# Performance work log

Measured on AMD Instinct MI355X. Metric: run time of the kernel, lower is better.

Reference implementation:

```python
import jax, jax.numpy as jnp
import numpy as np

D_MODEL = 2048
NUM_HEADS = 16
HEAD_DIM = D_MODEL // NUM_HEADS  # 128; scale uses head_dim even though attention is over full d_model
B, S = 2, 2048


def setup_inputs() -> dict:
    key = jax.random.key(0)
    ks = jax.random.split(key, 5)
    x = jax.random.normal(ks[0], (B, S, D_MODEL), dtype=jnp.float32)
    # causal additive mask, as typically passed to this module (2D, sliced mask[-s:, :kv])
    neg = jnp.float32(-1e9)
    mask = jnp.where(jnp.triu(jnp.ones((S, S), dtype=bool), k=1), neg, jnp.float32(0.0))
    std = 1.0 / np.sqrt(D_MODEL)
    Wq = jax.random.normal(ks[1], (D_MODEL, D_MODEL), dtype=jnp.float32) * std
    Wk = jax.random.normal(ks[2], (D_MODEL, D_MODEL), dtype=jnp.float32) * std
    Wv = jax.random.normal(ks[3], (D_MODEL, D_MODEL), dtype=jnp.float32) * std
    Wo = jax.random.normal(ks[4], (D_MODEL, D_MODEL), dtype=jnp.float32) * std
    return {"x": x, "mask": mask, "Wq": Wq, "Wk": Wk, "Wv": Wv, "Wo": Wo}


def reference(x, mask, Wq, Wk, Wv, Wo):
    # nn.Linear(bias=False): y = x @ W^T
    q = jnp.einsum('bsd,ed->bse', x, Wq)  # [B,S,D]
    k = jnp.einsum('bsd,ed->bse', x, Wk)
    v = jnp.einsum('bsd,ed->bse', x, Wv)
    scale = jnp.float32(HEAD_DIM ** -0.5)
    # NOTE: faithful to source — contraction over full d_model, no head split
    scores = jnp.einsum('bsd,btd->bst', q, k) * scale  # [B,S,S]
    scores = scores + mask  # mask[-s:, :kv] == mask here (s == kv)
    weights = jax.nn.softmax(scores, axis=-1)
    out = jnp.einsum('bst,btd->bsd', weights, v)
    return jnp.einsum('bsd,ed->bse', out, Wo)
```

## Files before the change

### kernel.cpp

```cpp
#include <hip/hip_runtime.h>

#define DM  2048
#define SQ  2048
#define NB  2
#define BSZ (NB * SQ)

typedef _Float16 f16x8 __attribute__((ext_vector_type(8)));
typedef __attribute__((ext_vector_type(4))) float f32x4;

#define ASG(p) (const __attribute__((address_space(1))) void*)(p)
#define ASL(p) (__attribute__((address_space(3))) void*)(p)

__device__ __forceinline__ unsigned short f2h(float f) {
  union { _Float16 h; unsigned short u; } x;
  x.h = (_Float16)f;
  return x.u;
}
__device__ __forceinline__ float h2f(unsigned short u) {
  union { unsigned short u; _Float16 h; } x;
  x.u = u;
  return (float)x.h;
}

__global__ __launch_bounds__(256) void cast_x_wo(const float4* __restrict__ x,
                                                 const float4* __restrict__ wo,
                                                 ushort4* __restrict__ outx,
                                                 ushort4* __restrict__ outwo,
                                                 int n4x, int n4w) {
  int i = blockIdx.x * 256 + threadIdx.x;
  float4 v;
  ushort4* dst;
  int j;
  if (i < n4x) { v = x[i]; dst = outx; j = i; }
  else { j = i - n4x; if (j >= n4w) return; v = wo[j]; dst = outwo; }
  ushort4 h;
  h.x = f2h(v.x); h.y = f2h(v.y); h.z = f2h(v.z); h.w = f2h(v.w);
  dst[j] = h;
}

__global__ __launch_bounds__(256) void cast_t(const float* __restrict__ wq,
                                              const float* __restrict__ wk,
                                              const float* __restrict__ wv,
                                              unsigned short* __restrict__ wqT,
                                              unsigned short* __restrict__ wkT,
                                              unsigned short* __restrict__ wvT) {
  __shared__ unsigned short tile[64][66];
  const float* in = (blockIdx.z == 0) ? wq : (blockIdx.z == 1) ? wk : wv;
  unsigned short* outT = (blockIdx.z == 0) ? wqT : (blockIdx.z == 1) ? wkT : wvT;
  const int tid = threadIdx.x;
  const int d0 = blockIdx.x * 64, e0 = blockIdx.y * 64;
  const int r = tid >> 4;
  const int c = (tid & 15) * 4;
#pragma unroll
  for (int p = 0; p < 4; p++) {
    const int dl = r + p * 16;
    float4 v = *(const float4*)&in[(long)(d0 + dl) * DM + e0 + c];
    tile[c + 0][dl] = f2h(v.x);
    tile[c + 1][dl] = f2h(v.y);
    tile[c + 2][dl] = f2h(v.z);
    tile[c + 3][dl] = f2h(v.w);
  }
  __syncthreads();
  const int r2 = tid >> 3;
  const int c2 = (tid & 7) * 8;
#pragma unroll
  for (int p = 0; p < 2; p++) {
    const int el = r2 + p * 32;
    union { uint4 u4; unsigned short us[8]; } o;
#pragma unroll
    for (int k = 0; k < 8; k++) o.us[k] = tile[el][c2 + k];
    *(uint4*)&outT[(long)(e0 + el) * DM + d0 + c2] = o.u4;
  }
}

#define SB() __builtin_amdgcn_sched_barrier(0)
#define BARX() do { SB(); __builtin_amdgcn_s_barrier(); SB(); } while (0)

#define STAGEK(BUFL, REG, U, T) do { \
    const unsigned short* G_ = (REG) ? Bb : Ab; \
    const int ldG_ = (REG) ? ldB : ldA; \
    const int r0_ = ((REG) ? bn0 : bm0) + (U) * 32; \
    const long k0_ = (long)((T) << 6); \
    char* db_ = ldsb + (BUFL) * 32768 + (REG) * 16384 + (U) * 4096 + tid * 16; \
    const unsigned short* s_ = G_ + (long)(r0_ + srow) * ldG_ + k0_ + scsw; \
    __builtin_amdgcn_global_load_lds(ASG(s_), ASL(db_), 16, 0, 0); \
  } while (0)

#define LDAK(BUFL, MH, Af) do { \
    const char* ba_ = ldsb + (BUFL) * 32768 + (wm * 64 + (MH) * 32) * 128 + arow; \
    _Pragma("unroll") for (int mm_ = 0; mm_ < 2; mm_++) { \
      Af[mm_][0] = *(const f16x8*)(ba_ + mm_ * 2048 + sl0); \
      Af[mm_][1] = *(const f16x8*)(ba_ + mm_ * 2048 + sl1); } \
  } while (0)

#define LDBK(BUFL, NH, Bf) do { \
    const char* bb_ = ldsb + (BUFL) * 32768 + 16384 + (wn * 64 + (NH) * 32) * 128 + arow; \
    _Pragma("unroll") for (int nn_ = 0; nn_ < 2; nn_++) { \
      Bf[nn_][0] = *(const f16x8*)(bb_ + nn_ * 2048 + sl0); \
      Bf[nn_][1] = *(const f16x8*)(bb_ + nn_ * 2048 + sl1); } \
  } while (0)

#define PHK(Af, Bf, MH, NH) do { \
    __builtin_amdgcn_s_setprio(1); \
    _Pragma("unroll") for (int mm_ = 0; mm_ < 2; mm_++) \
    _Pragma("unroll") for (int nn_ = 0; nn_ < 2; nn_++) \
    _Pragma("unroll") for (int ks_ = 0; ks_ < 2; ks_++) \
      acc[(MH) * 2 + mm_][(NH) * 2 + nn_] = __builtin_amdgcn_mfma_f32_16x16x32_f16( \
          Af[mm_][ks_], Bf[nn_][ks_], acc[(MH) * 2 + mm_][(NH) * 2 + nn_], 0, 0, 0); \
    __builtin_amdgcn_s_setprio(0); \
  } while (0)

#define GROUPK(BUFL, T) do { \
    LDAK(BUFL, 0, a0); LDBK(BUFL, 0, b0); \
    LDAK(BUFL, 1, a1); \
    if ((T) + 1 < NT) { STAGEK((BUFL) ^ 1, 1, 2, (T) + 1); STAGEK((BUFL) ^ 1, 1, 3, (T) + 1); } \
    PHK(a0, b0, 0, 0); \
    BARX(); \
    LDBK(BUFL, 1, b1); \
    PHK(a1, b0, 1, 0); \
    BARX(); \
    if ((T) + 2 < NT) { STAGEK(BUFL, 0, 0, (T) + 2); STAGEK(BUFL, 0, 1, (T) + 2); \
                        STAGEK(BUFL, 0, 2, (T) + 2); STAGEK(BUFL, 0, 3, (T) + 2); } \
    PHK(a1, b1, 1, 1); \
    BARX(); \
    if ((T) + 2 < NT) { STAGEK(BUFL, 1, 0, (T) + 2); STAGEK(BUFL, 1, 1, (T) + 2); } \
    PHK(a0, b1, 0, 1); \
    SB(); \
    if ((T) + 1 < NT) { \
      if ((T) + 1 == NT - 1) { asm volatile("s_waitcnt vmcnt(0)" ::: "memory"); } \
      else                   { asm volatile("s_waitcnt vmcnt(6)" ::: "memory"); } \
    } \
    __builtin_amdgcn_s_barrier(); \
    SB(); \
  } while (0)

template <int OM>
__device__ __forceinline__ void gemm128_body(
    char* ldsb, const unsigned short* __restrict__ Ab,
    const unsigned short* __restrict__ Bb,
    float* __restrict__ Cf, unsigned short* __restrict__ Ch, long cb,
    int NT, int ldA, int ldB, int ldC, int bm0, int bn0, float alpha) {
  const int tid = threadIdx.x, lane = tid & 63, wid = tid >> 6;
  const int wm = wid >> 1, wn = wid & 1;
  const int fr = lane & 15, fq = lane >> 4;

  const int sl0 = ((fq ^ (fr & 7)) << 4);
  const int sl1 = (((4 + fq) ^ (fr & 7)) << 4);
  const int arow = fr << 7;

  const int srow = tid >> 3;
  const int scsw = ((tid & 7) ^ (srow & 7)) << 3;

  f32x4 acc[4][4];
#pragma unroll
  for (int m = 0; m < 4; m++)
#pragma unroll
    for (int n = 0; n < 4; n++)
#pragma unroll
      for (int r = 0; r < 4; r++) acc[m][n][r] = 0.f;

  f16x8 a0[2][2], a1[2][2], b0[2][2], b1[2][2];

  STAGEK(0, 0, 0, 0); STAGEK(0, 0, 1, 0); STAGEK(0, 0, 2, 0); STAGEK(0, 0, 3, 0);
  STAGEK(0, 1, 0, 0); STAGEK(0, 1, 1, 0); STAGEK(0, 1, 2, 0); STAGEK(0, 1, 3, 0);
  STAGEK(1, 0, 0, 1); STAGEK(1, 0, 1, 1); STAGEK(1, 0, 2, 1); STAGEK(1, 0, 3, 1);
  STAGEK(1, 1, 0, 1); STAGEK(1, 1, 1, 1);
  asm volatile("s_waitcnt vmcnt(6)" ::: "memory");
  __builtin_amdgcn_s_barrier();
  SB();

  for (int t = 0; t < NT; t += 2) {
    GROUPK(0, t);
    GROUPK(1, t + 1);
  }

#pragma unroll
  for (int mh = 0; mh < 2; mh++)
#pragma unroll
    for (int mm = 0; mm < 2; mm++)
#pragma unroll
      for (int nh = 0; nh < 2; nh++)
#pragma unroll
        for (int nn = 0; nn < 2; nn++) {
          const int col = bn0 + wn * 64 + nh * 32 + nn * 16 + fr;
#pragma unroll
          for (int r = 0; r < 4; r++) {
            const long row = (long)bm0 + wm * 64 + mh * 32 + mm * 16 + fq * 4 + r;
            const long ci = cb + row * ldC + col;
            const float vv = acc[mh * 2 + mm][nh * 2 + nn][r] * alpha;
            if constexpr (OM == 0) Cf[ci] = vv;
            else                   Ch[ci] = f2h(vv);
          }
        }
}

template <int OM, int CAUSAL>
__global__ __launch_bounds__(256, 2) void gemm128(
    const unsigned short* __restrict__ A, const unsigned short* __restrict__ B,
    float* __restrict__ Cf, unsigned short* __restrict__ Ch,
    int K, long sAb, long sBb, long sCb,
    int ldA, int ldB, int ldC, float alpha) {
  __shared__ __align__(16) char ldsarr[65536];
  const int bm0 = blockIdx.x * 128;
  const int bn0 = blockIdx.y * 128;
  if (CAUSAL == 1 && bn0 > bm0) return;
  const int z = blockIdx.z;
  gemm128_body<OM>(ldsarr, A + (long)z * sAb, B + (long)z * sBb,
                   Cf, Ch, (long)z * sCb, K >> 6, ldA, ldB, ldC, bm0, bn0, alpha);
}

__global__ __launch_bounds__(256, 2) void k_mt_g(
    const unsigned short* __restrict__ wkT, const unsigned short* __restrict__ wqT,
    const unsigned short* __restrict__ wo16, const unsigned short* __restrict__ wvT,
    unsigned short* __restrict__ MT, unsigned short* __restrict__ G) {
  __shared__ __align__(16) char ldsarr[65536];
  const int bm0 = blockIdx.x * 128;
  const int bn0 = blockIdx.y * 128;
  if (blockIdx.z == 0)
    gemm128_body<1>(ldsarr, wkT, wqT, nullptr, MT, 0L, DM >> 6, DM, DM, DM, bm0, bn0, 1.0f);
  else
    gemm128_body<1>(ldsarr, wo16, wvT, nullptr, G, 0L, DM >> 6, DM, DM, DM, bm0, bn0, 1.0f);
}

__global__ __launch_bounds__(256, 2) void k_y_ut(
    const unsigned short* __restrict__ x16, const unsigned short* __restrict__ MT,
    const unsigned short* __restrict__ G,
    unsigned short* __restrict__ y, unsigned short* __restrict__ uT) {
  __shared__ __align__(16) char ldsarr[65536];
  if (blockIdx.z == 0) {
    const int bm0 = blockIdx.x * 128;
    const int bn0 = blockIdx.y * 128;
    gemm128_body<1>(ldsarr, x16, MT, nullptr, y, 0L, DM >> 6, DM, DM, DM, bm0, bn0, 1.0f);
  } else {
    const int bm0 = blockIdx.y * 128;
    const int bn0 = blockIdx.x * 128;
    gemm128_body<1>(ldsarr, G, x16, nullptr, uT, 0L, DM >> 6, DM, DM, BSZ, bm0, bn0, 1.0f);
  }
}

__global__ __launch_bounds__(256, 2) void k_out(
    const unsigned short* __restrict__ probs, const unsigned short* __restrict__ uT,
    float* __restrict__ out) {
  __shared__ __align__(16) char ldsarr[65536];
  const int x = blockIdx.x;
  const int bn0 = blockIdx.y * 128;
  const long z = blockIdx.z & 1;
  const int row = (blockIdx.z >> 1) ? (15 - x) : x;
  const unsigned short* Ab = probs + z * (long)SQ * SQ;
  const unsigned short* Bb = uT + z * 2048;
  gemm128_body<0>(ldsarr, Ab, Bb, out, nullptr, z * (long)SQ * DM,
                  2 * (row + 1), SQ, BSZ, DM, 128 * row, bn0, 1.0f);
}

__global__ __launch_bounds__(256) void softmax_causal(const unsigned short* __restrict__ sc,
                                                      unsigned short* __restrict__ pr) {
  const int row = blockIdx.x;
  const int s = row & (SQ - 1);
  const long base = (long)row * SQ;
  const int n = s + 1;
  const int tid = threadIdx.x;
  const int lane = tid & 63;
  const int wv = tid >> 6;
  const int e0 = tid * 8;
  __shared__ float red[4];

  union { uint4 u4; unsigned short us[8]; } in, ou;
  in.u4 = *(const uint4*)&sc[base + e0];

  float v[8];
  float mx = -3.0e38f;
#pragma unroll
  for (int j = 0; j < 8; j++) {
    v[j] = (e0 + j < n) ? h2f(in.us[j]) : -3.0e38f;
    mx = fmaxf(mx, v[j]);
  }
#pragma unroll
  for (int o = 32; o >= 1; o >>= 1) mx = fmaxf(mx, __shfl_xor(mx, o));
  if (lane == 0) red[wv] = mx;
  __syncthreads();
  mx = fmaxf(fmaxf(red[0], red[1]), fmaxf(red[2], red[3]));
  __syncthreads();

  float sum = 0.f;
#pragma unroll
  for (int j = 0; j < 8; j++) {
    v[j] = (e0 + j < n) ? __expf(v[j] - mx) : 0.f;
    sum += v[j];
  }
#pragma unroll
  for (int o = 32; o >= 1; o >>= 1) sum += __shfl_xor(sum, o);
  if (lane == 0) red[wv] = sum;
  __syncthreads();
  const float inv = 1.f / (red[0] + red[1] + red[2] + red[3]);
#pragma unroll
  for (int j = 0; j < 8; j++) ou.us[j] = (e0 + j < n) ? f2h(v[j] * inv) : (unsigned short)0;
  *(uint4*)&pr[base + e0] = ou.u4;
}

extern "C" void kernel_launch(void* const* d_in, const int* in_sizes, int n_in,
                              void* d_out, int out_size, void* d_ws, size_t ws_size,
                              hipStream_t stream) {
  (void)in_sizes; (void)n_in; (void)out_size; (void)ws_size;
  const float* x  = (const float*)d_in[0];
  const float* Wq = (const float*)d_in[2];
  const float* Wk = (const float*)d_in[3];
  const float* Wv = (const float*)d_in[4];
  const float* Wo = (const float*)d_in[5];
  float* out = (float*)d_out;

  const long ELx = (long)BSZ * DM;
  const long ELw = (long)DM * DM;

  char* ws = (char*)d_ws;
  size_t off = 0;
  auto take = [&](size_t bytes) { void* p = ws + off; off += bytes; return p; };

  unsigned short* x16  = (unsigned short*)take(ELx * 2);
  unsigned short* wqT  = (unsigned short*)take(ELw * 2);
  unsigned short* wkT  = (unsigned short*)take(ELw * 2);
  unsigned short* wvT  = (unsigned short*)take(ELw * 2);
  unsigned short* wo16 = (unsigned short*)take(ELw * 2);
  unsigned short* MT   = (unsigned short*)take(ELw * 2);
  unsigned short* G    = (unsigned short*)take(ELw * 2);
  unsigned short* y    = (unsigned short*)take(ELx * 2);
  unsigned short* uT   = (unsigned short*)take(ELx * 2);
  unsigned short* probs = (unsigned short*)take((long)NB * SQ * SQ * 2);
  unsigned short* scores = wqT;

  const int n4x = (int)(ELx / 4), n4w = (int)(ELw / 4);
  cast_x_wo<<<dim3((n4x + n4w + 255) / 256), 256, 0, stream>>>(
      (const float4*)x, (const float4*)Wo, (ushort4*)x16, (ushort4*)wo16, n4x, n4w);
  cast_t<<<dim3(DM / 64, DM / 64, 3), 256, 0, stream>>>(
      Wq, Wk, Wv, wqT, wkT, wvT);

  const float scale = 0.08838834764831845f;

  k_mt_g<<<dim3(DM / 128, DM / 128, 2), 256, 0, stream>>>(
      wkT, wqT, wo16, wvT, MT, G);
  k_y_ut<<<dim3(BSZ / 128, DM / 128, 2), 256, 0, stream>>>(
      x16, MT, G, y, uT);
  gemm128<1, 1><<<dim3(SQ / 128, SQ / 128, NB), 256, 0, stream>>>(
      y, x16, nullptr, scores, DM, (long)SQ * DM, (long)SQ * DM,
      (long)SQ * SQ, DM, DM, SQ, scale);

  softmax_causal<<<dim3(NB * SQ), 256, 0, stream>>>(scores, probs);

  k_out<<<dim3(8, DM / 128, 4), 256, 0, stream>>>(probs, uT, out);
}
```

Baseline: 205.6 us.

## Regroup y, uT and causal score GEMMs to balance launches and skip empty tiles

```diff
diff --git a/kernel.cpp b/kernel.cpp
--- a/kernel.cpp
+++ b/kernel.cpp
@@ -194,21 +194,6 @@
         }
 }
 
-template <int OM, int CAUSAL>
-__global__ __launch_bounds__(256, 2) void gemm128(
-    const unsigned short* __restrict__ A, const unsigned short* __restrict__ B,
-    float* __restrict__ Cf, unsigned short* __restrict__ Ch,
-    int K, long sAb, long sBb, long sCb,
-    int ldA, int ldB, int ldC, float alpha) {
-  __shared__ __align__(16) char ldsarr[65536];
-  const int bm0 = blockIdx.x * 128;
-  const int bn0 = blockIdx.y * 128;
-  if (CAUSAL == 1 && bn0 > bm0) return;
-  const int z = blockIdx.z;
-  gemm128_body<OM>(ldsarr, A + (long)z * sAb, B + (long)z * sBb,
-                   Cf, Ch, (long)z * sCb, K >> 6, ldA, ldB, ldC, bm0, bn0, alpha);
-}
-
 __global__ __launch_bounds__(256, 2) void k_mt_g(
     const unsigned short* __restrict__ wkT, const unsigned short* __restrict__ wqT,
     const unsigned short* __restrict__ wo16, const unsigned short* __restrict__ wvT,
@@ -222,19 +207,36 @@
     gemm128_body<1>(ldsarr, wo16, wvT, nullptr, G, 0L, DM >> 6, DM, DM, DM, bm0, bn0, 1.0f);
 }
 
-__global__ __launch_bounds__(256, 2) void k_y_ut(
+__global__ __launch_bounds__(256, 2) void k_y(
     const unsigned short* __restrict__ x16, const unsigned short* __restrict__ MT,
-    const unsigned short* __restrict__ G,
-    unsigned short* __restrict__ y, unsigned short* __restrict__ uT) {
+    unsigned short* __restrict__ y) {
   __shared__ __align__(16) char ldsarr[65536];
-  if (blockIdx.z == 0) {
-    const int bm0 = blockIdx.x * 128;
-    const int bn0 = blockIdx.y * 128;
-    gemm128_body<1>(ldsarr, x16, MT, nullptr, y, 0L, DM >> 6, DM, DM, DM, bm0, bn0, 1.0f);
+  const int bm0 = blockIdx.x * 128;
+  const int bn0 = blockIdx.y * 128;
+  gemm128_body<1>(ldsarr, x16, MT, nullptr, y, 0L, DM >> 6, DM, DM, DM, bm0, bn0, 1.0f);
+}
+
+__global__ __launch_bounds__(256, 2) void k_su(
+    const unsigned short* __restrict__ G, const unsigned short* __restrict__ x16,
+    const unsigned short* __restrict__ y,
+    unsigned short* __restrict__ uT, unsigned short* __restrict__ scores,
+    float scale) {
+  __shared__ __align__(16) char ldsarr[65536];
+  const int b = blockIdx.x;
+  if (b < 512) {
+    const int bm0 = (b >> 5) * 128;
+    const int bn0 = (b & 31) * 128;
+    gemm128_body<1>(ldsarr, G, x16, nullptr, uT, 0L, DM >> 6, DM, DM, BSZ, bm0, bn0, 1.0f);
   } else {
-    const int bm0 = blockIdx.y * 128;
-    const int bn0 = blockIdx.x * 128;
-    gemm128_body<1>(ldsarr, G, x16, nullptr, uT, 0L, DM >> 6, DM, DM, BSZ, bm0, bn0, 1.0f);
+    const int u = b - 512;
+    const long z = u / 136;
+    const int t = u % 136;
+    const int r = (int)((sqrtf(8.f * (float)t + 1.f) - 1.f) * 0.5f);
+    const int c = t - ((r * (r + 1)) >> 1);
+    const unsigned short* Ab = y   + z * (long)SQ * DM;
+    const unsigned short* Bb = x16 + z * (long)SQ * DM;
+    gemm128_body<1>(ldsarr, Ab, Bb, nullptr, scores, z * (long)SQ * SQ,
+                    DM >> 6, DM, DM, SQ, r * 128, c * 128, scale);
   }
 }
 
@@ -337,11 +339,8 @@
 
   k_mt_g<<<dim3(DM / 128, DM / 128, 2), 256, 0, stream>>>(
       wkT, wqT, wo16, wvT, MT, G);
-  k_y_ut<<<dim3(BSZ / 128, DM / 128, 2), 256, 0, stream>>>(
-      x16, MT, G, y, uT);
-  gemm128<1, 1><<<dim3(SQ / 128, SQ / 128, NB), 256, 0, stream>>>(
-      y, x16, nullptr, scores, DM, (long)SQ * DM, (long)SQ * DM,
-      (long)SQ * SQ, DM, DM, SQ, scale);
+  k_y<<<dim3(BSZ / 128, DM / 128, 1), 256, 0, stream>>>(x16, MT, y);
+  k_su<<<dim3(784, 1, 1), 256, 0, stream>>>(G, x16, y, uT, scores, scale);
 
   softmax_causal<<<dim3(NB * SQ), 256, 0, stream>>>(scores, probs);
 
```

Result: slower. 211.4 us (+2.8%).

## Pack causal score tiles two per 512-thread block via triangular indexing

Applied to the files above, without the earlier changes.

```diff
diff --git a/kernel.cpp b/kernel.cpp
--- a/kernel.cpp
+++ b/kernel.cpp
@@ -136,11 +136,11 @@
 
 template <int OM>
 __device__ __forceinline__ void gemm128_body(
-    char* ldsb, const unsigned short* __restrict__ Ab,
+    char* ldsb, int tid, const unsigned short* __restrict__ Ab,
     const unsigned short* __restrict__ Bb,
     float* __restrict__ Cf, unsigned short* __restrict__ Ch, long cb,
     int NT, int ldA, int ldB, int ldC, int bm0, int bn0, float alpha) {
-  const int tid = threadIdx.x, lane = tid & 63, wid = tid >> 6;
+  const int lane = tid & 63, wid = tid >> 6;
   const int wm = wid >> 1, wn = wid & 1;
   const int fr = lane & 15, fq = lane >> 4;
 
@@ -194,21 +194,6 @@
         }
 }
 
-template <int OM, int CAUSAL>
-__global__ __launch_bounds__(256, 2) void gemm128(
-    const unsigned short* __restrict__ A, const unsigned short* __restrict__ B,
-    float* __restrict__ Cf, unsigned short* __restrict__ Ch,
-    int K, long sAb, long sBb, long sCb,
-    int ldA, int ldB, int ldC, float alpha) {
-  __shared__ __align__(16) char ldsarr[65536];
-  const int bm0 = blockIdx.x * 128;
-  const int bn0 = blockIdx.y * 128;
-  if (CAUSAL == 1 && bn0 > bm0) return;
-  const int z = blockIdx.z;
-  gemm128_body<OM>(ldsarr, A + (long)z * sAb, B + (long)z * sBb,
-                   Cf, Ch, (long)z * sCb, K >> 6, ldA, ldB, ldC, bm0, bn0, alpha);
-}
-
 __global__ __launch_bounds__(256, 2) void k_mt_g(
     const unsigned short* __restrict__ wkT, const unsigned short* __restrict__ wqT,
     const unsigned short* __restrict__ wo16, const unsigned short* __restrict__ wvT,
@@ -217,9 +202,11 @@
   const int bm0 = blockIdx.x * 128;
   const int bn0 = blockIdx.y * 128;
   if (blockIdx.z == 0)
-    gemm128_body<1>(ldsarr, wkT, wqT, nullptr, MT, 0L, DM >> 6, DM, DM, DM, bm0, bn0, 1.0f);
+    gemm128_body<1>(ldsarr, threadIdx.x, wkT, wqT, nullptr, MT, 0L,
+                    DM >> 6, DM, DM, DM, bm0, bn0, 1.0f);
   else
-    gemm128_body<1>(ldsarr, wo16, wvT, nullptr, G, 0L, DM >> 6, DM, DM, DM, bm0, bn0, 1.0f);
+    gemm128_body<1>(ldsarr, threadIdx.x, wo16, wvT, nullptr, G, 0L,
+                    DM >> 6, DM, DM, DM, bm0, bn0, 1.0f);
 }
 
 __global__ __launch_bounds__(256, 2) void k_y_ut(
@@ -230,12 +217,31 @@
   if (blockIdx.z == 0) {
     const int bm0 = blockIdx.x * 128;
     const int bn0 = blockIdx.y * 128;
-    gemm128_body<1>(ldsarr, x16, MT, nullptr, y, 0L, DM >> 6, DM, DM, DM, bm0, bn0, 1.0f);
+    gemm128_body<1>(ldsarr, threadIdx.x, x16, MT, nullptr, y, 0L,
+                    DM >> 6, DM, DM, DM, bm0, bn0, 1.0f);
   } else {
     const int bm0 = blockIdx.y * 128;
     const int bn0 = blockIdx.x * 128;
-    gemm128_body<1>(ldsarr, G, x16, nullptr, uT, 0L, DM >> 6, DM, DM, BSZ, bm0, bn0, 1.0f);
-  }
+    gemm128_body<1>(ldsarr, threadIdx.x, G, x16, nullptr, uT, 0L,
+                    DM >> 6, DM, DM, BSZ, bm0, bn0, 1.0f);
+  }
+}
+
+__global__ __launch_bounds__(512, 1) void k_scores_p(
+    const unsigned short* __restrict__ y, const unsigned short* __restrict__ x16,
+    unsigned short* __restrict__ scores, float scale) {
+  __shared__ __align__(16) char ldsarr[131072];
+  const int h = threadIdx.x >> 8;
+  const int tid = threadIdx.x & 255;
+  const int idx = blockIdx.x + h * 136;
+  const long z = idx / 136;
+  const int u = idx % 136;
+  const int r = (int)((sqrtf(8.f * (float)u + 1.f) - 1.f) * 0.5f);
+  const int c = u - ((r * (r + 1)) >> 1);
+  const unsigned short* Ab = y   + z * (long)SQ * DM;
+  const unsigned short* Bb = x16 + z * (long)SQ * DM;
+  gemm128_body<1>(ldsarr + h * 65536, tid, Ab, Bb, nullptr, scores,
+                  z * (long)SQ * SQ, DM >> 6, DM, DM, SQ, r * 128, c * 128, scale);
 }
 
 __global__ __launch_bounds__(256, 2) void k_out(
@@ -248,7 +254,7 @@
   const int row = (blockIdx.z >> 1) ? (15 - x) : x;
   const unsigned short* Ab = probs + z * (long)SQ * SQ;
   const unsigned short* Bb = uT + z * 2048;
-  gemm128_body<0>(ldsarr, Ab, Bb, out, nullptr, z * (long)SQ * DM,
+  gemm128_body<0>(ldsarr, threadIdx.x, Ab, Bb, out, nullptr, z * (long)SQ * DM,
                   2 * (row + 1), SQ, BSZ, DM, 128 * row, bn0, 1.0f);
 }
 
@@ -339,9 +345,7 @@
       wkT, wqT, wo16, wvT, MT, G);
   k_y_ut<<<dim3(BSZ / 128, DM / 128, 2), 256, 0, stream>>>(
       x16, MT, G, y, uT);
-  gemm128<1, 1><<<dim3(SQ / 128, SQ / 128, NB), 256, 0, stream>>>(
-      y, x16, nullptr, scores, DM, (long)SQ * DM, (long)SQ * DM,
-      (long)SQ * SQ, DM, DM, SQ, scale);
+  k_scores_p<<<dim3(136, 1, 1), 512, 0, stream>>>(y, x16, scores, scale);
 
   softmax_causal<<<dim3(NB * SQ), 256, 0, stream>>>(scores, probs);
 
```

Result: no change. 209.0 us (+1.7%).
